# Kernel tuning notes

Measured on AMD Instinct MI355X. Metric: run time of the kernel, lower is better.

Reference implementation:

```python
import jax, jax.numpy as jnp
import numpy as np


def setup_inputs() -> dict:
    key = jax.random.key(0)
    k1, k2, k3 = jax.random.split(key, 3)
    B, C, H, W = 8, 256, 128, 128
    G, P = 1024, 1024
    sample_map = jax.random.normal(k1, (B, C, H, W), dtype=jnp.float32)
    sample_pts = jax.random.uniform(k2, (G, P, 2), dtype=jnp.float32)
    batch_ids = jax.random.randint(k3, (G,), 0, B, dtype=jnp.int64)
    return {"sample_map": sample_map, "sample_pts": sample_pts, "batch_ids": batch_ids}


def reference(sample_map, sample_pts, batch_ids):
    # Faithful to MapSampler2d: per-group batch gather + F.grid_sample
    # (bilinear, padding_mode='zeros', align_corners=False on pts mapped to [-1,1]).
    B, C, H, W = sample_map.shape
    bid = batch_ids.astype(jnp.int32)

    g = 2.0 * sample_pts - 1.0                      # [G,P,2] in [-1,1]
    # align_corners=False unnormalization
    x = (g[..., 0] + 1.0) * (W * 0.5) - 0.5          # [G,P]
    y = (g[..., 1] + 1.0) * (H * 0.5) - 0.5

    x0f = jnp.floor(x)
    y0f = jnp.floor(y)
    wx = x - x0f                                     # [G,P]
    wy = y - y0f
    x0 = x0f.astype(jnp.int32)
    y0 = y0f.astype(jnp.int32)

    map_hwc = jnp.transpose(sample_map, (0, 2, 3, 1))  # [B,H,W,C]

    def gather(yi, xi):
        # zeros padding: out-of-bounds corners contribute 0
        valid = (yi >= 0) & (yi < H) & (xi >= 0) & (xi < W)
        yc = jnp.clip(yi, 0, H - 1)
        xc = jnp.clip(xi, 0, W - 1)
        v = map_hwc[bid[:, None], yc, xc]            # [G,P,C]
        return v * valid[..., None].astype(v.dtype)

    v00 = gather(y0, x0)
    v01 = gather(y0, x0 + 1)
    v10 = gather(y0 + 1, x0)
    v11 = gather(y0 + 1, x0 + 1)

    wx_ = wx[..., None]
    wy_ = wy[..., None]
    out = (v00 * (1.0 - wx_) * (1.0 - wy_)
           + v01 * wx_ * (1.0 - wy_)
           + v10 * (1.0 - wx_) * wy_
           + v11 * wx_ * wy_)                        # [G,P,C]
    return out
```

## Files before the change

### kernel.cpp

```cpp
#include <hip/hip_runtime.h>

#define Bv 8
#define Cv 256
#define Hv 128
#define Wv 128
#define HWv (Hv * Wv)
#define Gv 1024
#define Pv 1024

typedef __attribute__((ext_vector_type(4))) _Float16 half4;
typedef __attribute__((ext_vector_type(4))) float f32x4;

#define META_INTS (1024 + 8 + 8 + 9)
#define MAP_OFF_BYTES 8192

__global__ __launch_bounds__(256) void transpose_h_k(const float* __restrict__ in,
                                                     _Float16* __restrict__ out) {
    __shared__ float tile[64][33];
    int b  = blockIdx.z;
    int c0 = blockIdx.y * 64;
    int s0 = blockIdx.x * 32;
    int lin = threadIdx.x;
    int tx  = lin & 31;
    int ty  = lin >> 5;

    const float* ip = in + ((size_t)(b * Cv + c0 + ty)) * HWv + s0 + tx;
#pragma unroll
    for (int i = 0; i < 64; i += 8)
        tile[ty + i][tx] = ip[(size_t)i * HWv];
    __syncthreads();

    int cp = lin & 31;
    int r8 = lin >> 5;
#pragma unroll
    for (int it = 0; it < 4; ++it) {
        int r = r8 + it * 8;
        union { _Float16 h[2]; unsigned u; } pk;
        pk.h[0] = (_Float16)tile[2 * cp + 0][r];
        pk.h[1] = (_Float16)tile[2 * cp + 1][r];
        unsigned* dst = (unsigned*)(out + ((size_t)b * HWv + s0 + r) * Cv + c0);
        dst[cp] = pk.u;
    }
}

__global__ __launch_bounds__(1024) void prep_k(const int* __restrict__ bids,
                                               int* __restrict__ meta) {
    __shared__ int hist[8], base[8];
    int t = threadIdx.x;
    if (t < 8) hist[t] = 0;
    __syncthreads();
    int b = bids[t] & 7;
    int rank = atomicAdd(&hist[b], 1);
    __syncthreads();
    if (t == 0) {
        int acc = 0;
#pragma unroll
        for (int j = 0; j < 8; ++j) { base[j] = acc; acc += hist[j]; }
        int blk = 0;
#pragma unroll
        for (int j = 0; j <= 8; ++j) {
            meta[1040 + j] = blk;
            if (j < 8) blk += hist[j] * 256;
        }
    }
    __syncthreads();
    meta[base[b] + rank] = t;
    if (t < 8) {
        meta[1024 + t] = hist[t];
        meta[1032 + t] = base[t];
    }
}

__global__ __launch_bounds__(256) void sample_loc_k(const _Float16* __restrict__ map,
                                                    const float* __restrict__ pts,
                                                    const int* __restrict__ meta,
                                                    float* __restrict__ out) {
    const int* perm = meta;
    const int* cnt  = meta + 1024;
    const int* off  = meta + 1032;
    const int* cum  = meta + 1040;

    int s = blockIdx.x;
    int j = 0;
#pragma unroll
    for (int k = 1; k < 8; ++k) j += (s >= cum[k]) ? 1 : 0;
    int r = s - cum[j];
    int W = cnt[j] << 7;
    int h = (r >= W) ? 1 : 0;
    r -= h * W;
    int gi = r >> 7, chunk = r & 127;
    int g = perm[off[j] + gi];

    int t    = threadIdx.x;
    int wv   = t >> 6;
    int lane = t & 63;
    int hl   = lane & 31;
    int which = lane >> 5;
    int pt = (g << 10) + (chunk << 3) + (wv << 1) + which;

    float px = pts[2 * (size_t)pt + 0];
    float py = pts[2 * (size_t)pt + 1];

    float x = (float)Wv * px - 0.5f;
    float y = (float)Hv * py - 0.5f;
    float x0f = floorf(x), y0f = floorf(y);
    float wx = x - x0f, wy = y - y0f;
    int x0 = (int)x0f, y0 = (int)y0f;
    int x1 = x0 + 1,   y1 = y0 + 1;

    bool vx0 = (unsigned)x0 < (unsigned)Wv;
    bool vx1 = (unsigned)x1 < (unsigned)Wv;
    bool vy0 = (unsigned)y0 < (unsigned)Hv;
    bool vy1 = (unsigned)y1 < (unsigned)Hv;
    int xc0 = min(max(x0, 0), Wv - 1);
    int xc1 = min(max(x1, 0), Wv - 1);
    int yc0 = min(max(y0, 0), Hv - 1);
    int yc1 = min(max(y1, 0), Hv - 1);

    float w00 = (1.0f - wx) * (1.0f - wy) * ((vx0 & vy0) ? 1.0f : 0.0f);
    float w01 = wx * (1.0f - wy)          * ((vx1 & vy0) ? 1.0f : 0.0f);
    float w10 = (1.0f - wx) * wy          * ((vx0 & vy1) ? 1.0f : 0.0f);
    float w11 = wx * wy                   * ((vx1 & vy1) ? 1.0f : 0.0f);

    size_t bbase = (size_t)j * HWv * Cv;
    size_t o00 = bbase + ((size_t)yc0 * Wv + xc0) * Cv;
    size_t o01 = bbase + ((size_t)yc0 * Wv + xc1) * Cv;
    size_t o10 = bbase + ((size_t)yc1 * Wv + xc0) * Cv;
    size_t o11 = bbase + ((size_t)yc1 * Wv + xc1) * Cv;

    int c0 = (h << 7) + (hl << 2);

    half4 v00 = *(const half4*)(map + o00 + c0);
    half4 v01 = *(const half4*)(map + o01 + c0);
    half4 v10 = *(const half4*)(map + o10 + c0);
    half4 v11 = *(const half4*)(map + o11 + c0);

    f32x4 rr;
    rr.x = (float)v00.x * w00 + (float)v01.x * w01 + (float)v10.x * w10 + (float)v11.x * w11;
    rr.y = (float)v00.y * w00 + (float)v01.y * w01 + (float)v10.y * w10 + (float)v11.y * w11;
    rr.z = (float)v00.z * w00 + (float)v01.z * w01 + (float)v10.z * w10 + (float)v11.z * w11;
    rr.w = (float)v00.w * w00 + (float)v01.w * w01 + (float)v10.w * w10 + (float)v11.w * w11;

    __builtin_nontemporal_store(rr, (f32x4*)(out + (size_t)pt * Cv + c0));
}

__global__ __launch_bounds__(256) void sample_nchw_k(const float* __restrict__ map,
                                                     const float* __restrict__ pts,
                                                     const int* __restrict__ bids,
                                                     float* __restrict__ out) {
    int t    = blockIdx.x * 256 + threadIdx.x;
    int pt   = t >> 6;
    int lane = t & 63;

    int g = pt >> 10;
    float px = pts[2 * (size_t)pt + 0];
    float py = pts[2 * (size_t)pt + 1];
    int b = bids[g];
    float x = (float)Wv * px - 0.5f;
    float y = (float)Hv * py - 0.5f;
    float x0f = floorf(x), y0f = floorf(y);
    float wx = x - x0f, wy = y - y0f;
    int x0 = (int)x0f, y0 = (int)y0f;
    int x1 = x0 + 1,   y1 = y0 + 1;
    bool vx0 = (unsigned)x0 < (unsigned)Wv;
    bool vx1 = (unsigned)x1 < (unsigned)Wv;
    bool vy0 = (unsigned)y0 < (unsigned)Hv;
    bool vy1 = (unsigned)y1 < (unsigned)Hv;
    int xc0 = min(max(x0, 0), Wv - 1);
    int xc1 = min(max(x1, 0), Wv - 1);
    int yc0 = min(max(y0, 0), Hv - 1);
    int yc1 = min(max(y1, 0), Hv - 1);
    float w00 = (1.0f - wx) * (1.0f - wy) * ((vx0 & vy0) ? 1.0f : 0.0f);
    float w01 = wx * (1.0f - wy)          * ((vx1 & vy0) ? 1.0f : 0.0f);
    float w10 = (1.0f - wx) * wy          * ((vx0 & vy1) ? 1.0f : 0.0f);
    float w11 = wx * wy                   * ((vx1 & vy1) ? 1.0f : 0.0f);

    int c = lane * 4;
    const float* base = map + ((size_t)b * Cv + c) * HWv;
    size_t s00 = (size_t)yc0 * Wv + xc0;
    size_t s01 = (size_t)yc0 * Wv + xc1;
    size_t s10 = (size_t)yc1 * Wv + xc0;
    size_t s11 = (size_t)yc1 * Wv + xc1;

    f32x4 r;
#pragma unroll
    for (int jj = 0; jj < 4; ++jj) {
        const float* ch = base + (size_t)jj * HWv;
        r[jj] = ch[s00] * w00 + ch[s01] * w01 + ch[s10] * w10 + ch[s11] * w11;
    }
    *((f32x4*)(out + (size_t)pt * Cv) + lane) = r;
}

extern "C" void kernel_launch(void* const* d_in, const int* in_sizes, int n_in,
                              void* d_out, int out_size, void* d_ws, size_t ws_size,
                              hipStream_t stream) {
    const float* map  = (const float*)d_in[0];
    const float* pts  = (const float*)d_in[1];
    const int*   bids = (const int*)d_in[2];
    float*       out  = (float*)d_out;

    size_t need = MAP_OFF_BYTES + (size_t)Bv * HWv * Cv * sizeof(_Float16);
    int npts = Gv * Pv;

    if (ws_size >= need) {
        int*      meta = (int*)d_ws;
        _Float16* nhwc = (_Float16*)((char*)d_ws + MAP_OFF_BYTES);

        prep_k<<<1, 1024, 0, stream>>>(bids, meta);
        transpose_h_k<<<dim3(HWv / 32, Cv / 64, Bv), 256, 0, stream>>>(map, nhwc);

        int nblocks = 256 * Gv;
        sample_loc_k<<<nblocks, 256, 0, stream>>>(nhwc, pts, meta, out);
    } else {
        int nblocks = npts * 64 / 256;
        sample_nchw_k<<<nblocks, 256, 0, stream>>>(map, pts, bids, out);
    }
}
```

Baseline: 307.0 us.

## Map sampling blocks to XCDs by batch to localize L2 reuse

Reorders the block-to-work mapping so that blocks landing on the same XCD (blockIdx mod 8) mostly process groups from a single batch image. Each XCD's L2 then caches one batch's NHWC fp16 map rather than all eight. Overflow from batches with more than an equal share of work is spread across the XCDs with spare slots. This relies on round-robin dispatch of blocks across the 8 XCDs, and the index computation adds a small per-block lookup.

```diff
diff --git a/kernel.cpp b/kernel.cpp
--- a/kernel.cpp
+++ b/kernel.cpp
@@ -7,11 +7,12 @@
 #define HWv (Hv * Wv)
 #define Gv 1024
 #define Pv 1024
+#define NBLK (256 * Gv)
+#define SLOTS (NBLK / 8)
 
 typedef __attribute__((ext_vector_type(4))) _Float16 half4;
 typedef __attribute__((ext_vector_type(4))) float f32x4;
 
-#define META_INTS (1024 + 8 + 8 + 9)
 #define MAP_OFF_BYTES 8192
 
 __global__ __launch_bounds__(256) void transpose_h_k(const float* __restrict__ in,
@@ -56,40 +57,55 @@
         int acc = 0;
 #pragma unroll
         for (int j = 0; j < 8; ++j) { base[j] = acc; acc += hist[j]; }
-        int blk = 0;
-#pragma unroll
-        for (int j = 0; j <= 8; ++j) {
-            meta[1040 + j] = blk;
-            if (j < 8) blk += hist[j] * 256;
+        int pl = 0, pe = 0;
+#pragma unroll
+        for (int j = 0; j < 8; ++j) {
+            int W = hist[j] * 256;
+            meta[1024 + j] = hist[j];
+            meta[1032 + j] = base[j];
+            meta[1040 + j] = W;
+            meta[1048 + j] = pl;
+            meta[1056 + j] = pe;
+            pl += max(0, SLOTS - W);
+            pe += max(0, W - SLOTS);
         }
     }
     __syncthreads();
     meta[base[b] + rank] = t;
-    if (t < 8) {
-        meta[1024 + t] = hist[t];
-        meta[1032 + t] = base[t];
-    }
-}
-
-__global__ __launch_bounds__(256) void sample_loc_k(const _Float16* __restrict__ map,
+}
+
+__global__ __launch_bounds__(256) void sample_xcd_k(const _Float16* __restrict__ map,
                                                     const float* __restrict__ pts,
                                                     const int* __restrict__ meta,
                                                     float* __restrict__ out) {
     const int* perm = meta;
     const int* cnt  = meta + 1024;
     const int* off  = meta + 1032;
-    const int* cum  = meta + 1040;
-
-    int s = blockIdx.x;
-    int j = 0;
-#pragma unroll
-    for (int k = 1; k < 8; ++k) j += (s >= cum[k]) ? 1 : 0;
-    int r = s - cum[j];
-    int W = cnt[j] << 7;
-    int h = (r >= W) ? 1 : 0;
-    r -= h * W;
-    int gi = r >> 7, chunk = r & 127;
-    int g = perm[off[j] + gi];
+    const int* Wq   = meta + 1040;
+    const int* PL   = meta + 1048;
+    const int* PE   = meta + 1056;
+
+    int bid = blockIdx.x;
+    int k = bid & 7;
+    int s = bid >> 3;
+
+    int j, i;
+    int Wk = Wq[k];
+    if (s < Wk) {
+        j = k; i = s;
+    } else {
+        int r = PL[k] + (s - Wk);
+        j = 0;
+#pragma unroll
+        for (int q = 1; q < 8; ++q) j += (r >= PE[q]) ? 1 : 0;
+        i = SLOTS + (r - PE[j]);
+    }
+
+    int half_items = cnt[j] << 7;
+    int h  = (i >= half_items) ? 1 : 0;
+    int rr = i - h * half_items;
+    int gi = rr >> 7, chunk = rr & 127;
+    int g  = perm[off[j] + gi];
 
     int t    = threadIdx.x;
     int wv   = t >> 6;
@@ -135,13 +151,13 @@
     half4 v10 = *(const half4*)(map + o10 + c0);
     half4 v11 = *(const half4*)(map + o11 + c0);
 
-    f32x4 rr;
-    rr.x = (float)v00.x * w00 + (float)v01.x * w01 + (float)v10.x * w10 + (float)v11.x * w11;
-    rr.y = (float)v00.y * w00 + (float)v01.y * w01 + (float)v10.y * w10 + (float)v11.y * w11;
-    rr.z = (float)v00.z * w00 + (float)v01.z * w01 + (float)v10.z * w10 + (float)v11.z * w11;
-    rr.w = (float)v00.w * w00 + (float)v01.w * w01 + (float)v10.w * w10 + (float)v11.w * w11;
-
-    __builtin_nontemporal_store(rr, (f32x4*)(out + (size_t)pt * Cv + c0));
+    f32x4 rr2;
+    rr2.x = (float)v00.x * w00 + (float)v01.x * w01 + (float)v10.x * w10 + (float)v11.x * w11;
+    rr2.y = (float)v00.y * w00 + (float)v01.y * w01 + (float)v10.y * w10 + (float)v11.y * w11;
+    rr2.z = (float)v00.z * w00 + (float)v01.z * w01 + (float)v10.z * w10 + (float)v11.z * w11;
+    rr2.w = (float)v00.w * w00 + (float)v01.w * w01 + (float)v10.w * w10 + (float)v11.w * w11;
+
+    __builtin_nontemporal_store(rr2, (f32x4*)(out + (size_t)pt * Cv + c0));
 }
 
 __global__ __launch_bounds__(256) void sample_nchw_k(const float* __restrict__ map,
@@ -208,9 +224,7 @@
 
         prep_k<<<1, 1024, 0, stream>>>(bids, meta);
         transpose_h_k<<<dim3(HWv / 32, Cv / 64, Bv), 256, 0, stream>>>(map, nhwc);
-
-        int nblocks = 256 * Gv;
-        sample_loc_k<<<nblocks, 256, 0, stream>>>(nhwc, pts, meta, out);
+        sample_xcd_k<<<NBLK, 256, 0, stream>>>(nhwc, pts, meta, out);
     } else {
         int nblocks = npts * 64 / 256;
         sample_nchw_k<<<nblocks, 256, 0, stream>>>(map, pts, bids, out);
```

Measured after the change: 284.6 us. 1.08x faster.
